# Kernel optimization log

Hardware: AMD Instinct MI355X
Metric: run time of the kernel (lower is better)

## Reference

```python
import jax, jax.numpy as jnp
import numpy as np

BATCH, S, N_DIM, B_SIZE = 512, 66, 304, 128

def setup_inputs() -> dict:
    key = jax.random.key(0)
    kx, kw = jax.random.split(key)
    x = jax.random.normal(kx, (BATCH, S, N_DIM), dtype=jnp.float32)
    W = jax.random.normal(kw, (B_SIZE, N_DIM), dtype=jnp.float32) * (1.0 / np.sqrt(N_DIM))
    b = jnp.zeros((B_SIZE,), dtype=jnp.float32)
    return {"x": x, "W": W, "b": b}

def reference(x, W, b):
    # Linear projection into tree space: (batch, S, B_size)
    t = jnp.einsum('bsd,kd->bsk', x, W) + b
    # Pairwise squared distances over sentence positions, same math as
    # expand/transpose/subtract/pow(2)/sum in the torch module.
    diff = t[:, :, None, :] - t[:, None, :, :]        # (batch, S, S, B_size)
    return jnp.sum(diff * diff, axis=-1)               # (batch, S, S)
```

## Files before the change

### kernel.cpp

```cpp
#include <hip/hip_runtime.h>
#include <hip/hip_bf16.h>

#define NBATCH 512
#define NS 66
#define ND 304
#define NK 128

#define XROWS 80
#define XSTRIDE_B 640
#define XBYTES (XROWS * XSTRIDE_B)
#define TSTRIDE_B 256
#define TBYTES (XROWS * TSTRIDE_B)
#define NTHREADS 512

typedef __attribute__((ext_vector_type(8))) short bf16x8;
typedef __attribute__((ext_vector_type(4))) short s16x4;
typedef __attribute__((ext_vector_type(4))) float f32x4;

__device__ __forceinline__ short f2bf(float x) {
    return __builtin_bit_cast(short, __float2bfloat16(x));
}

__device__ const int TI_LUT[15] = {0,1,2,3,4, 0,0,0,0,1,1,1,2,2,3};
__device__ const int TJ_LUT[15] = {0,1,2,3,4, 1,2,3,4,2,3,4,3,4,4};

__global__ __launch_bounds__(NTHREADS, 4) void treeprobe_mfma(
    const float* __restrict__ x,
    const float* __restrict__ W,
    float* __restrict__ out)
{
    __shared__ __align__(16) char lds[XBYTES + TBYTES + 80 * 4];
    char* const t_lds = lds + XBYTES;
    float* const norms = (float*)(lds + XBYTES + TBYTES);

    const int tid   = threadIdx.x;
    const int batch = blockIdx.x;
    const int lane  = tid & 63;
    const int wv    = tid >> 6;
    const int lr    = lane & 15;
    const int lg    = lane >> 4;

    const float* __restrict__ xb = x + (size_t)batch * NS * ND;

    float4 aA[6];
#pragma unroll
    for (int i = 0; i < 6; ++i) {
        const int e = tid + i * NTHREADS;
        aA[i] = (e < 2640)
            ? *reinterpret_cast<const float4*>(xb + (e / 40) * ND + (e % 40) * 4)
            : make_float4(0.f, 0.f, 0.f, 0.f);
    }

    for (int i = tid; i < 560; i += NTHREADS) {
        const int row = 66 + i / 40;
        *reinterpret_cast<f32x4*>(lds + row * XSTRIDE_B + (i % 40) * 16) =
            (f32x4){0.f, 0.f, 0.f, 0.f};
    }
    for (int i = tid; i < 132; i += NTHREADS) {
        const int row = i >> 1;
        const int byte = (row * XSTRIDE_B + 608 + (i & 1) * 16) ^ ((row & 7) << 4);
        *reinterpret_cast<f32x4*>(lds + byte) = (f32x4){0.f, 0.f, 0.f, 0.f};
    }

    bf16x8 wfrag[10];
    {
        const int c = wv * 16 + lr;
        const float* __restrict__ wr = W + c * ND;
#pragma unroll
        for (int kk = 0; kk < 10; ++kk) {
            const int k0 = kk * 32 + lg * 8;
            bf16x8 f = {0, 0, 0, 0, 0, 0, 0, 0};
            if (k0 < ND) {
                const float4 p0 = *reinterpret_cast<const float4*>(wr + k0);
                const float4 p1 = *reinterpret_cast<const float4*>(wr + k0 + 4);
                f[0] = f2bf(p0.x); f[1] = f2bf(p0.y);
                f[2] = f2bf(p0.z); f[3] = f2bf(p0.w);
                f[4] = f2bf(p1.x); f[5] = f2bf(p1.y);
                f[6] = f2bf(p1.z); f[7] = f2bf(p1.w);
            }
            wfrag[kk] = f;
        }
    }

#pragma unroll
    for (int i = 0; i < 6; ++i) {
        const int e = tid + i * NTHREADS;
        if (e < 2640) {
            const int s = e / 40;
            const int f = (e % 40) * 4;
            const int byte = (s * XSTRIDE_B + f * 2) ^ ((s & 7) << 4);
            s16x4 sv;
            sv[0] = f2bf(aA[i].x); sv[1] = f2bf(aA[i].y);
            sv[2] = f2bf(aA[i].z); sv[3] = f2bf(aA[i].w);
            *reinterpret_cast<s16x4*>(lds + byte) = sv;
        }
    }

    float4 aB[5];
#pragma unroll
    for (int i = 0; i < 5; ++i) {
        const int e = tid + i * NTHREADS;
        aB[i] = (e < 2376)
            ? *reinterpret_cast<const float4*>(xb + (e / 36) * ND + 160 + (e % 36) * 4)
            : make_float4(0.f, 0.f, 0.f, 0.f);
    }
    __syncthreads();

    f32x4 acc[5];
#pragma unroll
    for (int st = 0; st < 5; ++st) acc[st] = (f32x4){0.f, 0.f, 0.f, 0.f};

#pragma unroll
    for (int kk = 0; kk < 5; ++kk) {
        bf16x8 a[5];
#pragma unroll
        for (int st = 0; st < 5; ++st) {
            const int row = st * 16 + lr;
            const int byte = (row * XSTRIDE_B + kk * 64 + lg * 16) ^ ((row & 7) << 4);
            a[st] = *reinterpret_cast<const bf16x8*>(lds + byte);
        }
#pragma unroll
        for (int st = 0; st < 5; ++st)
            acc[st] = __builtin_amdgcn_mfma_f32_16x16x32_bf16(
                wfrag[kk], a[st], acc[st], 0, 0, 0);
    }

#pragma unroll
    for (int i = 0; i < 5; ++i) {
        const int e = tid + i * NTHREADS;
        if (e < 2376) {
            const int s = e / 36;
            const int f = 160 + (e % 36) * 4;
            const int byte = (s * XSTRIDE_B + f * 2) ^ ((s & 7) << 4);
            s16x4 sv;
            sv[0] = f2bf(aB[i].x); sv[1] = f2bf(aB[i].y);
            sv[2] = f2bf(aB[i].z); sv[3] = f2bf(aB[i].w);
            *reinterpret_cast<s16x4*>(lds + byte) = sv;
        }
    }
    __syncthreads();

#pragma unroll
    for (int kk = 5; kk < 10; ++kk) {
        bf16x8 a[5];
#pragma unroll
        for (int st = 0; st < 5; ++st) {
            const int row = st * 16 + lr;
            const int byte = (row * XSTRIDE_B + kk * 64 + lg * 16) ^ ((row & 7) << 4);
            a[st] = *reinterpret_cast<const bf16x8*>(lds + byte);
        }
#pragma unroll
        for (int st = 0; st < 5; ++st)
            acc[st] = __builtin_amdgcn_mfma_f32_16x16x32_bf16(
                wfrag[kk], a[st], acc[st], 0, 0, 0);
    }

#pragma unroll
    for (int st = 0; st < 5; ++st) {
        const int s = st * 16 + lr;
        const int c0 = wv * 16 + lg * 4;
        const int byte = (s * TSTRIDE_B + c0 * 2) ^ ((s & 7) << 4);
        s16x4 sv;
        sv[0] = f2bf(acc[st][0]); sv[1] = f2bf(acc[st][1]);
        sv[2] = f2bf(acc[st][2]); sv[3] = f2bf(acc[st][3]);
        *reinterpret_cast<s16x4*>(t_lds + byte) = sv;
    }
    __syncthreads();

    const int idx0 = wv;
    const int idx1 = wv + 8;
    const int ti0 = TI_LUT[idx0], tj0 = TJ_LUT[idx0];

    f32x4 g0 = (f32x4){0.f, 0.f, 0.f, 0.f};
#pragma unroll
    for (int kk = 0; kk < 4; ++kk) {
        const int ra = ti0 * 16 + lr;
        const int ba = (ra * TSTRIDE_B + kk * 64 + lg * 16) ^ ((ra & 7) << 4);
        const int rb = tj0 * 16 + lr;
        const int bb = (rb * TSTRIDE_B + kk * 64 + lg * 16) ^ ((rb & 7) << 4);
        g0 = __builtin_amdgcn_mfma_f32_16x16x32_bf16(
            *reinterpret_cast<const bf16x8*>(t_lds + ba),
            *reinterpret_cast<const bf16x8*>(t_lds + bb), g0, 0, 0, 0);
    }
    if (wv < 5) {
#pragma unroll
        for (int r = 0; r < 4; ++r)
            if (lr == lg * 4 + r) norms[wv * 16 + lr] = g0[r];
    }

    f32x4 g1 = (f32x4){0.f, 0.f, 0.f, 0.f};
    int ti1 = 0, tj1 = 0;
    if (idx1 < 15) {
        ti1 = TI_LUT[idx1]; tj1 = TJ_LUT[idx1];
#pragma unroll
        for (int kk = 0; kk < 4; ++kk) {
            const int ra = ti1 * 16 + lr;
            const int ba = (ra * TSTRIDE_B + kk * 64 + lg * 16) ^ ((ra & 7) << 4);
            const int rb = tj1 * 16 + lr;
            const int bb = (rb * TSTRIDE_B + kk * 64 + lg * 16) ^ ((rb & 7) << 4);
            g1 = __builtin_amdgcn_mfma_f32_16x16x32_bf16(
                *reinterpret_cast<const bf16x8*>(t_lds + ba),
                *reinterpret_cast<const bf16x8*>(t_lds + bb), g1, 0, 0, 0);
        }
    }
    __syncthreads();

    float* __restrict__ ob = out + (size_t)batch * NS * NS;

    {
        const int j = tj0 * 16 + lr;
        const float nj = norms[j];
        float v[4];
#pragma unroll
        for (int r = 0; r < 4; ++r) {
            const int i = ti0 * 16 + lg * 4 + r;
            v[r] = norms[i] + nj - 2.f * g0[r];
            if (i < NS && j < NS) ob[i * NS + j] = v[r];
        }
        if (ti0 != tj0 && j < NS) {
#pragma unroll
            for (int r = 0; r < 4; ++r) {
                const int i = ti0 * 16 + lg * 4 + r;
                if (i < NS) ob[j * NS + i] = v[r];
            }
        }
    }
    if (idx1 < 15) {
        const int j = tj1 * 16 + lr;
        const float nj = norms[j];
        float v[4];
#pragma unroll
        for (int r = 0; r < 4; ++r) {
            const int i = ti1 * 16 + lg * 4 + r;
            v[r] = norms[i] + nj - 2.f * g1[r];
            if (i < NS && j < NS) ob[i * NS + j] = v[r];
        }
        if (j < NS) {
#pragma unroll
            for (int r = 0; r < 4; ++r) {
                const int i = ti1 * 16 + lg * 4 + r;
                if (i < NS) ob[j * NS + i] = v[r];
            }
        }
    }
}

extern "C" void kernel_launch(void* const* d_in, const int* in_sizes, int n_in,
                              void* d_out, int out_size, void* d_ws, size_t ws_size,
                              hipStream_t stream) {
    const float* x = (const float*)d_in[0];
    const float* W = (const float*)d_in[1];
    float* out = (float*)d_out;

    treeprobe_mfma<<<NBATCH, NTHREADS, 0, stream>>>(x, W, out);
}
```

Baseline: 20.82 us.

## Split fused kernel into projection and distance kernels via bf16 workspace

Splits the single per-batch kernel into two launches when workspace allows. The first projects half a batch's rows per block into a bf16 t buffer in global memory. The second computes the Gram tiles and distances, with each block taking half of the tile pairs. This doubles the block count and shrinks per-block LDS so more blocks can be resident, at the cost of an extra launch and a global round trip of t. It also vectorises the transposed output stores to float2 and drops the two-phase x staging in the fallback fused kernel.

Result: slower. 35.63 us (+71.2%).

```diff
diff --git a/kernel.cpp b/kernel.cpp
--- a/kernel.cpp
+++ b/kernel.cpp
@@ -6,13 +6,6 @@
 #define ND 304
 #define NK 128
 
-#define XROWS 80
-#define XSTRIDE_B 640
-#define XBYTES (XROWS * XSTRIDE_B)
-#define TSTRIDE_B 256
-#define TBYTES (XROWS * TSTRIDE_B)
-#define NTHREADS 512
-
 typedef __attribute__((ext_vector_type(8))) short bf16x8;
 typedef __attribute__((ext_vector_type(4))) short s16x4;
 typedef __attribute__((ext_vector_type(4))) float f32x4;
@@ -21,45 +14,41 @@
     return __builtin_bit_cast(short, __float2bfloat16(x));
 }
 
-__device__ const int TI_LUT[15] = {0,1,2,3,4, 0,0,0,0,1,1,1,2,2,3};
-__device__ const int TJ_LUT[15] = {0,1,2,3,4, 1,2,3,4,2,3,4,3,4,4};
-
-__global__ __launch_bounds__(NTHREADS, 4) void treeprobe_mfma(
+#define A_THREADS 512
+#define A_XSTRIDE 640
+#define A_XROWS 48
+#define A_XBYTES (A_XROWS * A_XSTRIDE)
+
+__global__ __launch_bounds__(A_THREADS, 4) void treeprobe_t(
     const float* __restrict__ x,
     const float* __restrict__ W,
-    float* __restrict__ out)
+    short* __restrict__ tg)
 {
-    __shared__ __align__(16) char lds[XBYTES + TBYTES + 80 * 4];
-    char* const t_lds = lds + XBYTES;
-    float* const norms = (float*)(lds + XBYTES + TBYTES);
+    __shared__ __align__(16) char lds[A_XBYTES];
 
     const int tid   = threadIdx.x;
-    const int batch = blockIdx.x;
+    const int bid   = blockIdx.x;
+    const int batch = bid >> 1;
+    const int half  = bid & 1;
     const int lane  = tid & 63;
     const int wv    = tid >> 6;
     const int lr    = lane & 15;
     const int lg    = lane >> 4;
 
-    const float* __restrict__ xb = x + (size_t)batch * NS * ND;
-
-    float4 aA[6];
-#pragma unroll
-    for (int i = 0; i < 6; ++i) {
-        const int e = tid + i * NTHREADS;
-        aA[i] = (e < 2640)
-            ? *reinterpret_cast<const float4*>(xb + (e / 40) * ND + (e % 40) * 4)
+    const int r0     = half * 48;
+    const int nreal  = half ? (NS - 48) : 48;
+    const int ntiles = half ? 2 : 3;
+    const int nE     = nreal * 76;
+
+    const float* __restrict__ xb = x + (size_t)batch * NS * ND + (size_t)r0 * ND;
+
+    float4 ax[8];
+#pragma unroll
+    for (int i = 0; i < 8; ++i) {
+        const int e = tid + i * A_THREADS;
+        ax[i] = (e < nE)
+            ? *reinterpret_cast<const float4*>(xb + (e / 76) * ND + (e % 76) * 4)
             : make_float4(0.f, 0.f, 0.f, 0.f);
-    }
-
-    for (int i = tid; i < 560; i += NTHREADS) {
-        const int row = 66 + i / 40;
-        *reinterpret_cast<f32x4*>(lds + row * XSTRIDE_B + (i % 40) * 16) =
-            (f32x4){0.f, 0.f, 0.f, 0.f};
-    }
-    for (int i = tid; i < 132; i += NTHREADS) {
-        const int row = i >> 1;
-        const int byte = (row * XSTRIDE_B + 608 + (i & 1) * 16) ^ ((row & 7) << 4);
-        *reinterpret_cast<f32x4*>(lds + byte) = (f32x4){0.f, 0.f, 0.f, 0.f};
     }
 
     bf16x8 wfrag[10];
@@ -82,56 +71,250 @@
         }
     }
 
+    for (int i = tid; i < nreal * 2; i += A_THREADS) {
+        const int ls = i >> 1;
+        const int byte = (ls * A_XSTRIDE + 608 + (i & 1) * 16) ^ ((ls & 7) << 4);
+        *reinterpret_cast<f32x4*>(lds + byte) = (f32x4){0.f, 0.f, 0.f, 0.f};
+    }
+    if (half) {
+        for (int i = tid; i < 14 * 40; i += A_THREADS) {
+            const int ls = 18 + i / 40;
+            *reinterpret_cast<f32x4*>(lds + ls * A_XSTRIDE + (i % 40) * 16) =
+                (f32x4){0.f, 0.f, 0.f, 0.f};
+        }
+    }
+
+#pragma unroll
+    for (int i = 0; i < 8; ++i) {
+        const int e = tid + i * A_THREADS;
+        if (e < nE) {
+            const int ls  = e / 76;
+            const int col = (e % 76) * 4;
+            const int byte = (ls * A_XSTRIDE + col * 2) ^ ((ls & 7) << 4);
+            s16x4 sv;
+            sv[0] = f2bf(ax[i].x); sv[1] = f2bf(ax[i].y);
+            sv[2] = f2bf(ax[i].z); sv[3] = f2bf(ax[i].w);
+            *reinterpret_cast<s16x4*>(lds + byte) = sv;
+        }
+    }
+    __syncthreads();
+
+    f32x4 acc[3];
+#pragma unroll
+    for (int mt = 0; mt < 3; ++mt) acc[mt] = (f32x4){0.f, 0.f, 0.f, 0.f};
+
+#pragma unroll
+    for (int kk = 0; kk < 10; ++kk) {
+        bf16x8 a[3];
+#pragma unroll
+        for (int mt = 0; mt < 3; ++mt) {
+            if (mt < ntiles) {
+                const int ls = mt * 16 + lr;
+                const int byte = (ls * A_XSTRIDE + kk * 64 + lg * 16) ^ ((ls & 7) << 4);
+                a[mt] = *reinterpret_cast<const bf16x8*>(lds + byte);
+            }
+        }
+#pragma unroll
+        for (int mt = 0; mt < 3; ++mt)
+            if (mt < ntiles)
+                acc[mt] = __builtin_amdgcn_mfma_f32_16x16x32_bf16(
+                    wfrag[kk], a[mt], acc[mt], 0, 0, 0);
+    }
+
+#pragma unroll
+    for (int mt = 0; mt < 3; ++mt) {
+        if (mt < ntiles) {
+            const int s = r0 + mt * 16 + lr;
+            if (s < NS) {
+                s16x4 sv;
+                sv[0] = f2bf(acc[mt][0]); sv[1] = f2bf(acc[mt][1]);
+                sv[2] = f2bf(acc[mt][2]); sv[3] = f2bf(acc[mt][3]);
+                *reinterpret_cast<s16x4*>(
+                    tg + ((size_t)batch * NS + s) * NK + wv * 16 + lg * 4) = sv;
+            }
+        }
+    }
+}
+
+#define B_THREADS 256
+#define T_STRIDE_B 256
+#define T_BYTES (80 * T_STRIDE_B)
+
+__device__ const int BI_LUT[2][10] = {{0,1,2,3,4, 0,0,0,0,1},
+                                      {0,1,2,3,4, 1,1,2,2,3}};
+__device__ const int BJ_LUT[2][10] = {{0,1,2,3,4, 1,2,3,4,2},
+                                      {0,1,2,3,4, 3,4,3,4,4}};
+
+__global__ __launch_bounds__(B_THREADS, 4) void treeprobe_out(
+    const short* __restrict__ tg,
+    float* __restrict__ out)
+{
+    __shared__ __align__(16) char t_lds[T_BYTES];
+    __shared__ float norms[80];
+
+    const int tid   = threadIdx.x;
+    const int bid   = blockIdx.x;
+    const int batch = bid >> 1;
+    const int h     = bid & 1;
+    const int lane  = tid & 63;
+    const int wv    = tid >> 6;
+    const int lr    = lane & 15;
+    const int lg    = lane >> 4;
+
+    for (int i = tid; i < 14 * 16; i += B_THREADS) {
+        const int s = 66 + i / 16;
+        *reinterpret_cast<f32x4*>(t_lds + s * T_STRIDE_B + (i % 16) * 16) =
+            (f32x4){0.f, 0.f, 0.f, 0.f};
+    }
+    const short* __restrict__ tb = tg + (size_t)batch * NS * NK;
+#pragma unroll
+    for (int i = 0; i < 5; ++i) {
+        const int e = tid + i * B_THREADS;
+        if (e < 1056) {
+            const int s = e / 16;
+            const int c = e % 16;
+            const bf16x8 v = *reinterpret_cast<const bf16x8*>(tb + s * NK + c * 8);
+            const int byte = (s * T_STRIDE_B + c * 16) ^ ((s & 7) << 4);
+            *reinterpret_cast<bf16x8*>(t_lds + byte) = v;
+        }
+    }
+    __syncthreads();
+
+    f32x4 g[3];
+    int ti[3], tj[3];
+    bool valid[3], isdiag[3];
+#pragma unroll
+    for (int si = 0; si < 3; ++si) {
+        const int pos = wv + si * 4;
+        valid[si]  = pos < 10;
+        g[si] = (f32x4){0.f, 0.f, 0.f, 0.f};
+        ti[si] = 0; tj[si] = 0; isdiag[si] = false;
+        if (valid[si]) {
+            ti[si] = BI_LUT[h][pos];
+            tj[si] = BJ_LUT[h][pos];
+            isdiag[si] = pos < 5;
+#pragma unroll
+            for (int kk = 0; kk < 4; ++kk) {
+                const int ra = ti[si] * 16 + lr;
+                const int ba = (ra * T_STRIDE_B + kk * 64 + lg * 16) ^ ((ra & 7) << 4);
+                const int rb = tj[si] * 16 + lr;
+                const int bb = (rb * T_STRIDE_B + kk * 64 + lg * 16) ^ ((rb & 7) << 4);
+                g[si] = __builtin_amdgcn_mfma_f32_16x16x32_bf16(
+                    *reinterpret_cast<const bf16x8*>(t_lds + ba),
+                    *reinterpret_cast<const bf16x8*>(t_lds + bb), g[si], 0, 0, 0);
+            }
+            if (isdiag[si]) {
+#pragma unroll
+                for (int r = 0; r < 4; ++r)
+                    if (lr == lg * 4 + r) norms[ti[si] * 16 + lr] = g[si][r];
+            }
+        }
+    }
+    __syncthreads();
+
+    float* __restrict__ ob = out + (size_t)batch * NS * NS;
+#pragma unroll
+    for (int si = 0; si < 3; ++si) {
+        if (valid[si]) {
+            const int j = tj[si] * 16 + lr;
+            const float nj = norms[j];
+            float v[4];
+#pragma unroll
+            for (int r = 0; r < 4; ++r) {
+                const int i_ = ti[si] * 16 + lg * 4 + r;
+                v[r] = norms[i_] + nj - 2.f * g[si][r];
+                if (i_ < NS && j < NS && (h == 0 || !isdiag[si]))
+                    ob[i_ * NS + j] = v[r];
+            }
+            if (!isdiag[si] && j < NS) {
+                const int i0 = ti[si] * 16 + lg * 4;
+                *reinterpret_cast<float2*>(ob + j * NS + i0)     = make_float2(v[0], v[1]);
+                *reinterpret_cast<float2*>(ob + j * NS + i0 + 2) = make_float2(v[2], v[3]);
+            }
+        }
+    }
+}
+
+#define F_THREADS 512
+#define F_XSTRIDE 640
+#define F_XBYTES (80 * F_XSTRIDE)
+#define F_TBYTES (80 * 256)
+
+__device__ const int TI_LUT[15] = {0,1,2,3,4, 0,0,0,0,1,1,1,2,2,3};
+__device__ const int TJ_LUT[15] = {0,1,2,3,4, 1,2,3,4,2,3,4,3,4,4};
+
+__global__ __launch_bounds__(F_THREADS, 4) void treeprobe_fused(
+    const float* __restrict__ x, const float* __restrict__ W,
+    float* __restrict__ out)
+{
+    __shared__ __align__(16) char lds[F_XBYTES + F_TBYTES + 80 * 4];
+    char* const t_lds = lds + F_XBYTES;
+    float* const norms = (float*)(lds + F_XBYTES + F_TBYTES);
+
+    const int tid = threadIdx.x, batch = blockIdx.x;
+    const int lane = tid & 63, wv = tid >> 6, lr = lane & 15, lg = lane >> 4;
+    const float* __restrict__ xb = x + (size_t)batch * NS * ND;
+
+    float4 aA[6], aB[5];
 #pragma unroll
     for (int i = 0; i < 6; ++i) {
-        const int e = tid + i * NTHREADS;
+        const int e = tid + i * F_THREADS;
+        aA[i] = (e < 2640)
+            ? *reinterpret_cast<const float4*>(xb + (e / 40) * ND + (e % 40) * 4)
+            : make_float4(0.f, 0.f, 0.f, 0.f);
+    }
+#pragma unroll
+    for (int i = 0; i < 5; ++i) {
+        const int e = tid + i * F_THREADS;
+        aB[i] = (e < 2376)
+            ? *reinterpret_cast<const float4*>(xb + (e / 36) * ND + 160 + (e % 36) * 4)
+            : make_float4(0.f, 0.f, 0.f, 0.f);
+    }
+    bf16x8 wfrag[10];
+    {
+        const int c = wv * 16 + lr;
+        const float* __restrict__ wr = W + c * ND;
+#pragma unroll
+        for (int kk = 0; kk < 10; ++kk) {
+            const int k0 = kk * 32 + lg * 8;
+            bf16x8 f = {0, 0, 0, 0, 0, 0, 0, 0};
+            if (k0 < ND) {
+                const float4 p0 = *reinterpret_cast<const float4*>(wr + k0);
+                const float4 p1 = *reinterpret_cast<const float4*>(wr + k0 + 4);
+                f[0] = f2bf(p0.x); f[1] = f2bf(p0.y); f[2] = f2bf(p0.z); f[3] = f2bf(p0.w);
+                f[4] = f2bf(p1.x); f[5] = f2bf(p1.y); f[6] = f2bf(p1.z); f[7] = f2bf(p1.w);
+            }
+            wfrag[kk] = f;
+        }
+    }
+    for (int i = tid; i < 560; i += F_THREADS) {
+        const int row = 66 + i / 40;
+        *reinterpret_cast<f32x4*>(lds + row * F_XSTRIDE + (i % 40) * 16) =
+            (f32x4){0.f, 0.f, 0.f, 0.f};
+    }
+    for (int i = tid; i < 132; i += F_THREADS) {
+        const int row = i >> 1;
+        const int byte = (row * F_XSTRIDE + 608 + (i & 1) * 16) ^ ((row & 7) << 4);
+        *reinterpret_cast<f32x4*>(lds + byte) = (f32x4){0.f, 0.f, 0.f, 0.f};
+    }
+#pragma unroll
+    for (int i = 0; i < 6; ++i) {
+        const int e = tid + i * F_THREADS;
         if (e < 2640) {
-            const int s = e / 40;
-            const int f = (e % 40) * 4;
-            const int byte = (s * XSTRIDE_B + f * 2) ^ ((s & 7) << 4);
+            const int s = e / 40, f = (e % 40) * 4;
+            const int byte = (s * F_XSTRIDE + f * 2) ^ ((s & 7) << 4);
             s16x4 sv;
             sv[0] = f2bf(aA[i].x); sv[1] = f2bf(aA[i].y);
             sv[2] = f2bf(aA[i].z); sv[3] = f2bf(aA[i].w);
             *reinterpret_cast<s16x4*>(lds + byte) = sv;
         }
     }
-
-    float4 aB[5];
 #pragma unroll
     for (int i = 0; i < 5; ++i) {
-        const int e = tid + i * NTHREADS;
-        aB[i] = (e < 2376)
-            ? *reinterpret_cast<const float4*>(xb + (e / 36) * ND + 160 + (e % 36) * 4)
-            : make_float4(0.f, 0.f, 0.f, 0.f);
-    }
-    __syncthreads();
-
-    f32x4 acc[5];
-#pragma unroll
-    for (int st = 0; st < 5; ++st) acc[st] = (f32x4){0.f, 0.f, 0.f, 0.f};
-
-#pragma unroll
-    for (int kk = 0; kk < 5; ++kk) {
-        bf16x8 a[5];
-#pragma unroll
-        for (int st = 0; st < 5; ++st) {
-            const int row = st * 16 + lr;
-            const int byte = (row * XSTRIDE_B + kk * 64 + lg * 16) ^ ((row & 7) << 4);
-            a[st] = *reinterpret_cast<const bf16x8*>(lds + byte);
-        }
-#pragma unroll
-        for (int st = 0; st < 5; ++st)
-            acc[st] = __builtin_amdgcn_mfma_f32_16x16x32_bf16(
-                wfrag[kk], a[st], acc[st], 0, 0, 0);
-    }
-
-#pragma unroll
-    for (int i = 0; i < 5; ++i) {
-        const int e = tid + i * NTHREADS;
+        const int e = tid + i * F_THREADS;
         if (e < 2376) {
-            const int s = e / 36;
-            const int f = 160 + (e % 36) * 4;
-            const int byte = (s * XSTRIDE_B + f * 2) ^ ((s & 7) << 4);
+            const int s = e / 36, f = 160 + (e % 36) * 4;
+            const int byte = (s * F_XSTRIDE + f * 2) ^ ((s & 7) << 4);
             s16x4 sv;
             sv[0] = f2bf(aB[i].x); sv[1] = f2bf(aB[i].y);
             sv[2] = f2bf(aB[i].z); sv[3] = f2bf(aB[i].w);
@@ -140,13 +323,16 @@
     }
     __syncthreads();
 
-#pragma unroll
-    for (int kk = 5; kk < 10; ++kk) {
+    f32x4 acc[5];
+#pragma unroll
+    for (int st = 0; st < 5; ++st) acc[st] = (f32x4){0.f, 0.f, 0.f, 0.f};
+#pragma unroll
+    for (int kk = 0; kk < 10; ++kk) {
         bf16x8 a[5];
 #pragma unroll
         for (int st = 0; st < 5; ++st) {
             const int row = st * 16 + lr;
-            const int byte = (row * XSTRIDE_B + kk * 64 + lg * 16) ^ ((row & 7) << 4);
+            const int byte = (row * F_XSTRIDE + kk * 64 + lg * 16) ^ ((row & 7) << 4);
             a[st] = *reinterpret_cast<const bf16x8*>(lds + byte);
         }
 #pragma unroll
@@ -154,12 +340,11 @@
             acc[st] = __builtin_amdgcn_mfma_f32_16x16x32_bf16(
                 wfrag[kk], a[st], acc[st], 0, 0, 0);
     }
-
 #pragma unroll
     for (int st = 0; st < 5; ++st) {
         const int s = st * 16 + lr;
         const int c0 = wv * 16 + lg * 4;
-        const int byte = (s * TSTRIDE_B + c0 * 2) ^ ((s & 7) << 4);
+        const int byte = (s * 256 + c0 * 2) ^ ((s & 7) << 4);
         s16x4 sv;
         sv[0] = f2bf(acc[st][0]); sv[1] = f2bf(acc[st][1]);
         sv[2] = f2bf(acc[st][2]); sv[3] = f2bf(acc[st][3]);
@@ -167,17 +352,15 @@
     }
     __syncthreads();
 
-    const int idx0 = wv;
-    const int idx1 = wv + 8;
+    const int idx0 = wv, idx1 = wv + 8;
     const int ti0 = TI_LUT[idx0], tj0 = TJ_LUT[idx0];
-
     f32x4 g0 = (f32x4){0.f, 0.f, 0.f, 0.f};
 #pragma unroll
     for (int kk = 0; kk < 4; ++kk) {
         const int ra = ti0 * 16 + lr;
-        const int ba = (ra * TSTRIDE_B + kk * 64 + lg * 16) ^ ((ra & 7) << 4);
+        const int ba = (ra * 256 + kk * 64 + lg * 16) ^ ((ra & 7) << 4);
         const int rb = tj0 * 16 + lr;
-        const int bb = (rb * TSTRIDE_B + kk * 64 + lg * 16) ^ ((rb & 7) << 4);
+        const int bb = (rb * 256 + kk * 64 + lg * 16) ^ ((rb & 7) << 4);
         g0 = __builtin_amdgcn_mfma_f32_16x16x32_bf16(
             *reinterpret_cast<const bf16x8*>(t_lds + ba),
             *reinterpret_cast<const bf16x8*>(t_lds + bb), g0, 0, 0, 0);
@@ -187,7 +370,6 @@
         for (int r = 0; r < 4; ++r)
             if (lr == lg * 4 + r) norms[wv * 16 + lr] = g0[r];
     }
-
     f32x4 g1 = (f32x4){0.f, 0.f, 0.f, 0.f};
     int ti1 = 0, tj1 = 0;
     if (idx1 < 15) {
@@ -195,9 +377,9 @@
 #pragma unroll
         for (int kk = 0; kk < 4; ++kk) {
             const int ra = ti1 * 16 + lr;
-            const int ba = (ra * TSTRIDE_B + kk * 64 + lg * 16) ^ ((ra & 7) << 4);
+            const int ba = (ra * 256 + kk * 64 + lg * 16) ^ ((ra & 7) << 4);
             const int rb = tj1 * 16 + lr;
-            const int bb = (rb * TSTRIDE_B + kk * 64 + lg * 16) ^ ((rb & 7) << 4);
+            const int bb = (rb * 256 + kk * 64 + lg * 16) ^ ((rb & 7) << 4);
             g1 = __builtin_amdgcn_mfma_f32_16x16x32_bf16(
                 *reinterpret_cast<const bf16x8*>(t_lds + ba),
                 *reinterpret_cast<const bf16x8*>(t_lds + bb), g1, 0, 0, 0);
@@ -206,7 +388,6 @@
     __syncthreads();
 
     float* __restrict__ ob = out + (size_t)batch * NS * NS;
-
     {
         const int j = tj0 * 16 + lr;
         const float nj = norms[j];
@@ -218,11 +399,9 @@
             if (i < NS && j < NS) ob[i * NS + j] = v[r];
         }
         if (ti0 != tj0 && j < NS) {
-#pragma unroll
-            for (int r = 0; r < 4; ++r) {
-                const int i = ti0 * 16 + lg * 4 + r;
-                if (i < NS) ob[j * NS + i] = v[r];
-            }
+            const int i0 = ti0 * 16 + lg * 4;
+            *reinterpret_cast<float2*>(ob + j * NS + i0)     = make_float2(v[0], v[1]);
+            *reinterpret_cast<float2*>(ob + j * NS + i0 + 2) = make_float2(v[2], v[3]);
         }
     }
     if (idx1 < 15) {
@@ -236,11 +415,9 @@
             if (i < NS && j < NS) ob[i * NS + j] = v[r];
         }
         if (j < NS) {
-#pragma unroll
-            for (int r = 0; r < 4; ++r) {
-                const int i = ti1 * 16 + lg * 4 + r;
-                if (i < NS) ob[j * NS + i] = v[r];
-            }
+            const int i0 = ti1 * 16 + lg * 4;
+            *reinterpret_cast<float2*>(ob + j * NS + i0)     = make_float2(v[0], v[1]);
+            *reinterpret_cast<float2*>(ob + j * NS + i0 + 2) = make_float2(v[2], v[3]);
         }
     }
 }
@@ -252,5 +429,12 @@
     const float* W = (const float*)d_in[1];
     float* out = (float*)d_out;
 
-    treeprobe_mfma<<<NBATCH, NTHREADS, 0, stream>>>(x, W, out);
+    const size_t t_bytes = (size_t)NBATCH * NS * NK * 2;
+    if (ws_size >= t_bytes) {
+        short* tg = (short*)d_ws;
+        treeprobe_t<<<NBATCH * 2, A_THREADS, 0, stream>>>(x, W, tg);
+        treeprobe_out<<<NBATCH * 2, B_THREADS, 0, stream>>>(tg, out);
+    } else {
+        treeprobe_fused<<<NBATCH, F_THREADS, 0, stream>>>(x, W, out);
+    }
 }
```
